# Performance work log

Hardware: AMD Instinct MI355X
Metric: run time of the kernel (lower is better)

The kernel has to match this reference:

```python
import jax, jax.numpy as jnp
import numpy as np

BLOCK = 16          # NVFP4 block size along contraction dim
FP4_MAX = 6.0       # max magnitude of E2M1
FP8_MAX = 448.0     # max magnitude of float8_e4m3fn

_LEVELS = jnp.array([0.0, 0.5, 1.0, 1.5, 2.0, 3.0, 4.0, 6.0], dtype=jnp.float32)
_MIDS   = jnp.array([0.25, 0.75, 1.25, 1.75, 2.5, 3.5, 5.0], dtype=jnp.float32)


def quantize_dequant_nvfp4(t, global_scale):
    """Fake-quantize t (last dim % 16 == 0) to NVFP4: per-16-block fp8-e4m3
    scale times global fp32 scale, values snapped to the E2M1 grid."""
    shp = t.shape
    tb = t.reshape(shp[:-1] + (shp[-1] // BLOCK, BLOCK))
    amax = jnp.max(jnp.abs(tb), axis=-1, keepdims=True)
    # per-block scale, quantized to float8_e4m3fn as in TensorCoreNVFP4Layout
    bs = amax / (FP4_MAX * global_scale)
    bs8 = bs.astype(jnp.float8_e4m3fn).astype(jnp.float32)
    scale = bs8 * global_scale                       # effective dequant scale
    v = tb / jnp.maximum(scale, 1e-12)
    sign = jnp.sign(v)
    a = jnp.clip(jnp.abs(v), 0.0, FP4_MAX)
    idx = jnp.sum(a[..., None] > _MIDS, axis=-1)     # nearest E2M1 level
    q = _LEVELS[idx] * sign * scale
    return q.reshape(shp)


def setup_inputs() -> dict:
    key = jax.random.key(0)
    kx, kw, kb = jax.random.split(key, 3)
    x = jax.random.normal(kx, (8192, 4096), dtype=jnp.float32)
    weight = jax.random.normal(kw, (4096, 4096), dtype=jnp.float32) * 0.02
    bias = jax.random.normal(kb, (4096,), dtype=jnp.float32) * 0.02
    # global scales (weight_scale_2 / input_scale): amax / (6 * 448)
    input_scale = jnp.max(jnp.abs(x)) / (FP4_MAX * FP8_MAX)
    weight_scale = jnp.max(jnp.abs(weight)) / (FP4_MAX * FP8_MAX)
    return {"x": x, "weight": weight, "bias": bias,
            "input_scale": input_scale, "weight_scale": weight_scale}


def reference(x, weight, bias, input_scale, weight_scale):
    xq = quantize_dequant_nvfp4(x, input_scale)      # [T, K]
    wq = quantize_dequant_nvfp4(weight, weight_scale)  # [N, K]
    return jnp.einsum('tk,nk->tn', xq, wq) + bias    # F.linear
```

## Files before the change

kernel.cpp:

```cpp
#include <hip/hip_runtime.h>
#include <hip/hip_bf16.h>
#include <stdint.h>

typedef __attribute__((ext_vector_type(8))) __bf16 bf16x8;
typedef __attribute__((ext_vector_type(4))) float f32x4;
typedef __attribute__((ext_vector_type(4))) unsigned int u32x4;

#define BM 256
#define BN 256
#define BKT 32
#define RING 4
#define SLOT_BYTES 16384


__device__ __forceinline__ float fp8_e4m3_rne(float x) {
  if (x < 0.015625f) {
    return rintf(x * 512.0f) * 0.001953125f;
  }
  uint32_t u = __float_as_uint(x);
  uint32_t keep = u & 0xFFF00000u;
  uint32_t rem  = u & 0x000FFFFFu;
  uint32_t lsb  = (u >> 20) & 1u;
  if (rem > 0x80000u || (rem == 0x80000u && lsb)) keep += 0x100000u;
  return __uint_as_float(keep);
}

__device__ __forceinline__ float snap_lvl(float a) {
  if (a > 5.0f)  return 6.0f;
  if (a > 3.5f)  return 4.0f;
  if (a > 2.5f)  return 3.0f;
  if (a > 1.75f) return 2.0f;
  if (a > 1.25f) return 1.5f;
  if (a > 0.75f) return 1.0f;
  if (a > 0.25f) return 0.5f;
  return 0.0f;
}

__global__ __launch_bounds__(256) void quant_nvfp4(
    const float* __restrict__ in, unsigned short* __restrict__ out,
    const float* __restrict__ gsp, int nblk) {
  int b = blockIdx.x * 256 + threadIdx.x;
  if (b >= nblk) return;
  float gs = gsp[0];
  const float4* p = reinterpret_cast<const float4*>(in) + (size_t)b * 4;
  float v[16];
#pragma unroll
  for (int i = 0; i < 4; ++i) {
    float4 t4 = p[i];
    v[i * 4 + 0] = t4.x; v[i * 4 + 1] = t4.y;
    v[i * 4 + 2] = t4.z; v[i * 4 + 3] = t4.w;
  }
  float amax = 0.0f;
#pragma unroll
  for (int i = 0; i < 16; ++i) amax = fmaxf(amax, fabsf(v[i]));
  float bs8 = fp8_e4m3_rne(amax / (6.0f * gs));
  float scale = fmaxf(bs8 * gs, 1e-12f);
  unsigned short o[16];
#pragma unroll
  for (int i = 0; i < 16; ++i) {
    float q = v[i] / scale;
    float a = fminf(fabsf(q), 6.0f);
    float val = copysignf(snap_lvl(a) * bs8, q);
    o[i] = (unsigned short)(__float_as_uint(val) >> 16);
  }
  uint4 w0 = make_uint4((uint32_t)o[0] | ((uint32_t)o[1] << 16),
                        (uint32_t)o[2] | ((uint32_t)o[3] << 16),
                        (uint32_t)o[4] | ((uint32_t)o[5] << 16),
                        (uint32_t)o[6] | ((uint32_t)o[7] << 16));
  uint4 w1 = make_uint4((uint32_t)o[8]  | ((uint32_t)o[9]  << 16),
                        (uint32_t)o[10] | ((uint32_t)o[11] << 16),
                        (uint32_t)o[12] | ((uint32_t)o[13] << 16),
                        (uint32_t)o[14] | ((uint32_t)o[15] << 16));
  uint4* op = reinterpret_cast<uint4*>(out + (size_t)b * 16);
  op[0] = w0;
  op[1] = w1;
}


__device__ __forceinline__ void async_lds16(const void* g, void* l) {
  __builtin_amdgcn_global_load_lds((__attribute__((address_space(1))) void*)(g),
                                   (__attribute__((address_space(3))) void*)(l),
                                   16, 0, 0);
}

#define DSR(dst, a) asm volatile("ds_read_b128 %0, %1" : "=v"(dst) : "v"(a))
#define LGKM(N) do { asm volatile("s_waitcnt lgkmcnt(" #N ")" ::: "memory"); \
                     __builtin_amdgcn_sched_barrier(0); } while (0)
#define BCB(x) __builtin_bit_cast(bf16x8, x)

#define MF4(mi, ar) do {                                                       \
    acc[mi][0] = __builtin_amdgcn_mfma_f32_16x16x32_bf16(BCB(ar), BCB(rb0), acc[mi][0], 0, 0, 0); \
    acc[mi][1] = __builtin_amdgcn_mfma_f32_16x16x32_bf16(BCB(ar), BCB(rb1), acc[mi][1], 0, 0, 0); \
    acc[mi][2] = __builtin_amdgcn_mfma_f32_16x16x32_bf16(BCB(ar), BCB(rb2), acc[mi][2], 0, 0, 0); \
    acc[mi][3] = __builtin_amdgcn_mfma_f32_16x16x32_bf16(BCB(ar), BCB(rb3), acc[mi][3], 0, 0, 0); \
  } while (0)

#define TILE(T, DO_STAGE, VMWAIT) do {                                         \
    const unsigned soff = (unsigned)(((T) & 3) * SLOT_BYTES);                  \
    VMWAIT;                                                                    \
    __builtin_amdgcn_s_barrier();                                              \
    if (DO_STAGE) {                                                            \
      char* _la = (char*)As + (((T) + 3) & 3) * SLOT_BYTES;                    \
      char* _lb = (char*)Bs + (((T) + 3) & 3) * SLOT_BYTES;                    \
      async_lds16(pA0 + (size_t)((T) + 3) * BKT, _la + lo0);                   \
      async_lds16(pB0 + (size_t)((T) + 3) * BKT, _lb + lo0);                   \
      async_lds16(pA1 + (size_t)((T) + 3) * BKT, _la + lo1);                   \
      async_lds16(pB1 + (size_t)((T) + 3) * BKT, _lb + lo1);                   \
    }                                                                          \
    u32x4 rb0, rb1, rb2, rb3, ra0, ra1, ra2, ra3, ra4, ra5, ra6, ra7;          \
    DSR(rb0, adB[0] + soff); DSR(rb1, adB[1] + soff);                          \
    DSR(rb2, adB[2] + soff); DSR(rb3, adB[3] + soff);                          \
    DSR(ra0, adA[0] + soff); DSR(ra1, adA[1] + soff);                          \
    DSR(ra2, adA[2] + soff); DSR(ra3, adA[3] + soff);                          \
    __builtin_amdgcn_sched_barrier(0);                                         \
    LGKM(3); __builtin_amdgcn_s_setprio(1); MF4(0, ra0);                       \
    LGKM(2); MF4(1, ra1);                                                      \
    __builtin_amdgcn_sched_barrier(0);                                         \
    DSR(ra4, adA[4] + soff); DSR(ra5, adA[5] + soff);                          \
    DSR(ra6, adA[6] + soff); DSR(ra7, adA[7] + soff);                          \
    __builtin_amdgcn_sched_barrier(0);                                         \
    LGKM(5); MF4(2, ra2);                                                      \
    LGKM(4); MF4(3, ra3);                                                      \
    LGKM(3); MF4(4, ra4);                                                      \
    LGKM(2); MF4(5, ra5);                                                      \
    LGKM(1); MF4(6, ra6);                                                      \
    LGKM(0); MF4(7, ra7);                                                      \
    __builtin_amdgcn_s_setprio(0);                                             \
    __builtin_amdgcn_sched_barrier(0);                                         \
  } while (0)

#define STAGE_TILE(s) {                                                        \
    char* _la = (char*)As + ((s) & 3) * SLOT_BYTES;                            \
    char* _lb = (char*)Bs + ((s) & 3) * SLOT_BYTES;                            \
    async_lds16(pA0 + (size_t)(s) * BKT, _la + lo0);                           \
    async_lds16(pB0 + (size_t)(s) * BKT, _lb + lo0);                           \
    async_lds16(pA1 + (size_t)(s) * BKT, _la + lo1);                           \
    async_lds16(pB1 + (size_t)(s) * BKT, _lb + lo1);                           \
  }

__global__ __launch_bounds__(512, 2) void gemm_bt_bf16(
    const unsigned short* __restrict__ A, const unsigned short* __restrict__ B,
    const float* __restrict__ bias, const float* __restrict__ gsx,
    const float* __restrict__ gsw, float* __restrict__ C,
    int M, int N, int K) {
  __shared__ __align__(16) unsigned short As[RING * 8192];
  __shared__ __align__(16) unsigned short Bs[RING * 8192];

  const int t = threadIdx.x;
  const int l = t & 63;
  const int w = t >> 6;
  const int wm = w >> 2, wn = w & 3;

  const int nbn = N / BN;
  const int nwg = (M / BM) * nbn;
  const int cpx = nwg >> 3;
  int bid = blockIdx.x;
  int logical = (bid & 7) * cpx + (bid >> 3);
  const int bm = logical / nbn, bn = logical % nbn;
  const int brow = bm * BM, bcol = bn * BN;

  unsigned int b0 = (unsigned int)t * 16u;
  unsigned int b1 = b0 + 8192u;
  unsigned int bp0 = b0 ^ (((b0 >> 7) & 3u) << 4);
  unsigned int bp1 = b1 ^ (((b1 >> 7) & 3u) << 4);
  const unsigned int lo0 = b0, lo1 = b1;
  const unsigned short* pA0 = A + (size_t)(brow + (bp0 >> 6)) * K + ((bp0 & 63u) >> 1);
  const unsigned short* pA1 = A + (size_t)(brow + (bp1 >> 6)) * K + ((bp1 & 63u) >> 1);
  const unsigned short* pB0 = B + (size_t)(bcol + (bp0 >> 6)) * K + ((bp0 & 63u) >> 1);
  const unsigned short* pB1 = B + (size_t)(bcol + (bp1 >> 6)) * K + ((bp1 & 63u) >> 1);

  const unsigned baseAu = (unsigned)(uintptr_t)(&As[0]);
  const unsigned baseBu = (unsigned)(uintptr_t)(&Bs[0]);
  unsigned int adA[8], adB[4];
#pragma unroll
  for (int mi = 0; mi < 8; ++mi) {
    unsigned int r = wm * 128 + mi * 16 + (l & 15);
    unsigned int q = r * 64 + ((l >> 4) << 4);
    adA[mi] = baseAu + (q ^ (((q >> 7) & 3u) << 4));
  }
#pragma unroll
  for (int ni = 0; ni < 4; ++ni) {
    unsigned int r = wn * 64 + ni * 16 + (l & 15);
    unsigned int q = r * 64 + ((l >> 4) << 4);
    adB[ni] = baseBu + (q ^ (((q >> 7) & 3u) << 4));
  }

  f32x4 acc[8][4] = {};

  const int nsub = K / BKT;

  STAGE_TILE(0);
  STAGE_TILE(1);
  STAGE_TILE(2);

#pragma unroll 1
  for (int T = 0; T < nsub - 3; ++T) {
    TILE(T, 1, asm volatile("s_waitcnt vmcnt(8)" ::: "memory"));
  }
  TILE(nsub - 3, 0, asm volatile("s_waitcnt vmcnt(8)" ::: "memory"));
  TILE(nsub - 2, 0, asm volatile("s_waitcnt vmcnt(4)" ::: "memory"));
  TILE(nsub - 1, 0, asm volatile("s_waitcnt vmcnt(0)" ::: "memory"));

  const float gscale = gsx[0] * gsw[0];
  float bias_r[4];
#pragma unroll
  for (int ni = 0; ni < 4; ++ni)
    bias_r[ni] = bias[bcol + wn * 64 + ni * 16 + (l & 15)];
#pragma unroll
  for (int mi = 0; mi < 8; ++mi) {
#pragma unroll
    for (int ni = 0; ni < 4; ++ni) {
#pragma unroll
      for (int r = 0; r < 4; ++r) {
        int row = brow + wm * 128 + mi * 16 + (l >> 4) * 4 + r;
        int col = bcol + wn * 64 + ni * 16 + (l & 15);
        C[(size_t)row * N + col] = acc[mi][ni][r] * gscale + bias_r[ni];
      }
    }
  }
}


extern "C" void kernel_launch(void* const* d_in, const int* in_sizes, int n_in,
                              void* d_out, int out_size, void* d_ws, size_t ws_size,
                              hipStream_t stream) {
  const float* x    = (const float*)d_in[0];
  const float* wgt  = (const float*)d_in[1];
  const float* bias = (const float*)d_in[2];
  const float* isc  = (const float*)d_in[3];
  const float* wsc  = (const float*)d_in[4];
  float* out = (float*)d_out;

  const int N = in_sizes[2];
  const int K = in_sizes[1] / N;
  const int M = in_sizes[0] / K;

  unsigned short* Aq = (unsigned short*)d_ws;
  unsigned short* Bq = Aq + (size_t)M * K;

  int nblkA = M * K / 16;
  quant_nvfp4<<<(nblkA + 255) / 256, 256, 0, stream>>>(x, Aq, isc, nblkA);
  int nblkB = N * K / 16;
  quant_nvfp4<<<(nblkB + 255) / 256, 256, 0, stream>>>(wgt, Bq, wsc, nblkB);

  dim3 grid((M / BM) * (N / BN));
  gemm_bt_bf16<<<grid, 512, 0, stream>>>(Aq, Bq, bias, isc, wsc, out, M, N, K);
}
```

Before: 290.8 us.

## Process two K-tiles per barrier with a five-slot LDS ring

Replaces the four-slot, one-tile-per-barrier main loop with a five-slot LDS ring where each barrier window stages two new tiles and computes two K sub-tiles, interleaving LDS reads of the second tile with MFMAs of the first. This halves the number of workgroup barriers and gives deeper software prefetch overlap. It raises LDS use to 320 KB-equivalent slots (160 KB per block), which may cut occupancy below the requested two blocks per CU. It also hardcodes K=4096 through the fixed trip count of 62 windows.

```diff
diff --git a/kernel.cpp b/kernel.cpp
--- a/kernel.cpp
+++ b/kernel.cpp
@@ -9,8 +9,7 @@
 #define BM 256
 #define BN 256
 #define BKT 32
-#define RING 4
-#define SLOT_BYTES 16384
+#define SLOT 16384
 
 
 __device__ __forceinline__ float fp8_e4m3_rne(float x) {
@@ -88,63 +87,71 @@
                      __builtin_amdgcn_sched_barrier(0); } while (0)
 #define BCB(x) __builtin_bit_cast(bf16x8, x)
 
-#define MF4(mi, ar) do {                                                       \
-    acc[mi][0] = __builtin_amdgcn_mfma_f32_16x16x32_bf16(BCB(ar), BCB(rb0), acc[mi][0], 0, 0, 0); \
-    acc[mi][1] = __builtin_amdgcn_mfma_f32_16x16x32_bf16(BCB(ar), BCB(rb1), acc[mi][1], 0, 0, 0); \
-    acc[mi][2] = __builtin_amdgcn_mfma_f32_16x16x32_bf16(BCB(ar), BCB(rb2), acc[mi][2], 0, 0, 0); \
-    acc[mi][3] = __builtin_amdgcn_mfma_f32_16x16x32_bf16(BCB(ar), BCB(rb3), acc[mi][3], 0, 0, 0); \
+#define MF4(mi, ar, b0, b1, b2, b3) do {                                       \
+    acc[mi][0] = __builtin_amdgcn_mfma_f32_16x16x32_bf16(BCB(ar), BCB(b0), acc[mi][0], 0, 0, 0); \
+    acc[mi][1] = __builtin_amdgcn_mfma_f32_16x16x32_bf16(BCB(ar), BCB(b1), acc[mi][1], 0, 0, 0); \
+    acc[mi][2] = __builtin_amdgcn_mfma_f32_16x16x32_bf16(BCB(ar), BCB(b2), acc[mi][2], 0, 0, 0); \
+    acc[mi][3] = __builtin_amdgcn_mfma_f32_16x16x32_bf16(BCB(ar), BCB(b3), acc[mi][3], 0, 0, 0); \
   } while (0)
 
-#define TILE(T, DO_STAGE, VMWAIT) do {                                         \
-    const unsigned soff = (unsigned)(((T) & 3) * SLOT_BYTES);                  \
-    VMWAIT;                                                                    \
+#define STAGE(tile, soff) {                                                    \
+    char* _la = (char*)As + (soff);                                            \
+    char* _lb = (char*)Bs + (soff);                                            \
+    async_lds16(pA0 + (size_t)(tile) * BKT, _la + lo0);                        \
+    async_lds16(pB0 + (size_t)(tile) * BKT, _lb + lo0);                        \
+    async_lds16(pA1 + (size_t)(tile) * BKT, _la + lo1);                        \
+    async_lds16(pB1 + (size_t)(tile) * BKT, _lb + lo1);                        \
+  }
+
+#define WINDOW(VMSTR, ta, oa, ob, o3, o4, DO3, DO4) do {                       \
+    u32x4 rb0, rb1, rb2, rb3, ra0, ra1, ra2, ra3, ra4, ra5, ra6, ra7;          \
+    u32x4 qb0, qb1, qb2, qb3, qa0, qa1, qa2, qa3, qa4, qa5, qa6, qa7;          \
+    asm volatile("s_waitcnt vmcnt(" VMSTR ")" ::: "memory");                   \
     __builtin_amdgcn_s_barrier();                                              \
-    if (DO_STAGE) {                                                            \
-      char* _la = (char*)As + (((T) + 3) & 3) * SLOT_BYTES;                    \
-      char* _lb = (char*)Bs + (((T) + 3) & 3) * SLOT_BYTES;                    \
-      async_lds16(pA0 + (size_t)((T) + 3) * BKT, _la + lo0);                   \
-      async_lds16(pB0 + (size_t)((T) + 3) * BKT, _lb + lo0);                   \
-      async_lds16(pA1 + (size_t)((T) + 3) * BKT, _la + lo1);                   \
-      async_lds16(pB1 + (size_t)((T) + 3) * BKT, _lb + lo1);                   \
-    }                                                                          \
-    u32x4 rb0, rb1, rb2, rb3, ra0, ra1, ra2, ra3, ra4, ra5, ra6, ra7;          \
-    DSR(rb0, adB[0] + soff); DSR(rb1, adB[1] + soff);                          \
-    DSR(rb2, adB[2] + soff); DSR(rb3, adB[3] + soff);                          \
-    DSR(ra0, adA[0] + soff); DSR(ra1, adA[1] + soff);                          \
-    DSR(ra2, adA[2] + soff); DSR(ra3, adA[3] + soff);                          \
-    __builtin_amdgcn_sched_barrier(0);                                         \
-    LGKM(3); __builtin_amdgcn_s_setprio(1); MF4(0, ra0);                       \
-    LGKM(2); MF4(1, ra1);                                                      \
-    __builtin_amdgcn_sched_barrier(0);                                         \
-    DSR(ra4, adA[4] + soff); DSR(ra5, adA[5] + soff);                          \
-    DSR(ra6, adA[6] + soff); DSR(ra7, adA[7] + soff);                          \
-    __builtin_amdgcn_sched_barrier(0);                                         \
-    LGKM(5); MF4(2, ra2);                                                      \
-    LGKM(4); MF4(3, ra3);                                                      \
-    LGKM(3); MF4(4, ra4);                                                      \
-    LGKM(2); MF4(5, ra5);                                                      \
-    LGKM(1); MF4(6, ra6);                                                      \
-    LGKM(0); MF4(7, ra7);                                                      \
+    if (DO3) STAGE((ta) + 3, o3);                                              \
+    if (DO4) STAGE((ta) + 4, o4);                                              \
+    DSR(rb0, adB[0] + (oa)); DSR(rb1, adB[1] + (oa));                          \
+    DSR(rb2, adB[2] + (oa)); DSR(rb3, adB[3] + (oa));                          \
+    DSR(ra0, adA[0] + (oa)); DSR(ra1, adA[1] + (oa));                          \
+    DSR(ra2, adA[2] + (oa)); DSR(ra3, adA[3] + (oa));                          \
+    DSR(ra4, adA[4] + (oa)); DSR(ra5, adA[5] + (oa));                          \
+    DSR(ra6, adA[6] + (oa)); DSR(ra7, adA[7] + (oa));                          \
+    __builtin_amdgcn_sched_barrier(0);                                         \
+    LGKM(7); __builtin_amdgcn_s_setprio(1); MF4(0, ra0, rb0, rb1, rb2, rb3);   \
+    LGKM(6); MF4(1, ra1, rb0, rb1, rb2, rb3);                                  \
+    LGKM(5); MF4(2, ra2, rb0, rb1, rb2, rb3);                                  \
+    LGKM(4); MF4(3, ra3, rb0, rb1, rb2, rb3);                                  \
+    LGKM(3); MF4(4, ra4, rb0, rb1, rb2, rb3);                                  \
+    DSR(qb0, adB[0] + (ob)); DSR(qb1, adB[1] + (ob));                          \
+    DSR(qb2, adB[2] + (ob)); DSR(qb3, adB[3] + (ob));                          \
+    DSR(qa0, adA[0] + (ob)); DSR(qa1, adA[1] + (ob));                          \
+    DSR(qa2, adA[2] + (ob)); DSR(qa3, adA[3] + (ob));                          \
+    __builtin_amdgcn_sched_barrier(0);                                         \
+    LGKM(10); MF4(5, ra5, rb0, rb1, rb2, rb3);                                 \
+    LGKM(9);  MF4(6, ra6, rb0, rb1, rb2, rb3);                                 \
+    LGKM(8);  MF4(7, ra7, rb0, rb1, rb2, rb3);                                 \
+    DSR(qa4, adA[4] + (ob)); DSR(qa5, adA[5] + (ob));                          \
+    DSR(qa6, adA[6] + (ob)); DSR(qa7, adA[7] + (ob));                          \
+    __builtin_amdgcn_sched_barrier(0);                                         \
+    LGKM(7); MF4(0, qa0, qb0, qb1, qb2, qb3);                                  \
+    LGKM(6); MF4(1, qa1, qb0, qb1, qb2, qb3);                                  \
+    LGKM(5); MF4(2, qa2, qb0, qb1, qb2, qb3);                                  \
+    LGKM(4); MF4(3, qa3, qb0, qb1, qb2, qb3);                                  \
+    LGKM(3); MF4(4, qa4, qb0, qb1, qb2, qb3);                                  \
+    LGKM(2); MF4(5, qa5, qb0, qb1, qb2, qb3);                                  \
+    LGKM(1); MF4(6, qa6, qb0, qb1, qb2, qb3);                                  \
+    LGKM(0); MF4(7, qa7, qb0, qb1, qb2, qb3);                                  \
     __builtin_amdgcn_s_setprio(0);                                             \
     __builtin_amdgcn_sched_barrier(0);                                         \
   } while (0)
-
-#define STAGE_TILE(s) {                                                        \
-    char* _la = (char*)As + ((s) & 3) * SLOT_BYTES;                            \
-    char* _lb = (char*)Bs + ((s) & 3) * SLOT_BYTES;                            \
-    async_lds16(pA0 + (size_t)(s) * BKT, _la + lo0);                           \
-    async_lds16(pB0 + (size_t)(s) * BKT, _lb + lo0);                           \
-    async_lds16(pA1 + (size_t)(s) * BKT, _la + lo1);                           \
-    async_lds16(pB1 + (size_t)(s) * BKT, _lb + lo1);                           \
-  }
 
 __global__ __launch_bounds__(512, 2) void gemm_bt_bf16(
     const unsigned short* __restrict__ A, const unsigned short* __restrict__ B,
     const float* __restrict__ bias, const float* __restrict__ gsx,
     const float* __restrict__ gsw, float* __restrict__ C,
     int M, int N, int K) {
-  __shared__ __align__(16) unsigned short As[RING * 8192];
-  __shared__ __align__(16) unsigned short Bs[RING * 8192];
+  __shared__ __align__(16) unsigned short As[5 * 8192];
+  __shared__ __align__(16) unsigned short Bs[5 * 8192];
 
   const int t = threadIdx.x;
   const int l = t & 63;
@@ -187,19 +194,22 @@
 
   f32x4 acc[8][4] = {};
 
-  const int nsub = K / BKT;
-
-  STAGE_TILE(0);
-  STAGE_TILE(1);
-  STAGE_TILE(2);
-
+  STAGE(0, 0);
+  STAGE(1, SLOT);
+  STAGE(2, 2 * SLOT);
+
+  int sa = 0;
 #pragma unroll 1
-  for (int T = 0; T < nsub - 3; ++T) {
-    TILE(T, 1, asm volatile("s_waitcnt vmcnt(8)" ::: "memory"));
-  }
-  TILE(nsub - 3, 0, asm volatile("s_waitcnt vmcnt(8)" ::: "memory"));
-  TILE(nsub - 2, 0, asm volatile("s_waitcnt vmcnt(4)" ::: "memory"));
-  TILE(nsub - 1, 0, asm volatile("s_waitcnt vmcnt(0)" ::: "memory"));
+  for (int k = 0; k < 62; ++k) {
+    int ta = 2 * k;
+    int sb = sa + 1; if (sb >= 5) sb -= 5;
+    int s3 = sa + 3; if (s3 >= 5) s3 -= 5;
+    int s4 = sa + 4; if (s4 >= 5) s4 -= 5;
+    WINDOW("4", ta, sa * SLOT, sb * SLOT, s3 * SLOT, s4 * SLOT, 1, 1);
+    sa += 2; if (sa >= 5) sa -= 5;
+  }
+  WINDOW("4", 124, 4 * SLOT, 0 * SLOT, 2 * SLOT, 0, 1, 0);
+  WINDOW("0", 126, 1 * SLOT, 2 * SLOT, 0, 0, 0, 0);
 
   const float gscale = gsx[0] * gsw[0];
   float bias_r[4];
```

Result: faster. 282.1 us (-3.0%).

## Switch GEMM main loop to 32x32x16 bf16 MFMA with five-slot LDS ring

Applied to the files above, without the earlier changes.

Replaces the 16x16x32 MFMA tiling (8x4 accumulators per wave) with 32x32x16 MFMA instructions (8 f32x16 accumulators), remapping LDS read addresses and the epilogue output row/col mapping. This cuts the number of MFMA issues per tile. The LDS ring grows from 4 to 5 slots while keeping a prefetch distance of 3, with slot indices tracked by a rolling counter. The K loop count is hardcoded to 125 iterations, which assumes K=4096. The larger LDS footprint may constrain occupancy.

```diff
diff --git a/kernel.cpp b/kernel.cpp
--- a/kernel.cpp
+++ b/kernel.cpp
@@ -3,14 +3,13 @@
 #include <stdint.h>
 
 typedef __attribute__((ext_vector_type(8))) __bf16 bf16x8;
-typedef __attribute__((ext_vector_type(4))) float f32x4;
+typedef __attribute__((ext_vector_type(16))) float f32x16;
 typedef __attribute__((ext_vector_type(4))) unsigned int u32x4;
 
 #define BM 256
 #define BN 256
 #define BKT 32
-#define RING 4
-#define SLOT_BYTES 16384
+#define SLOT 16384
 
 
 __device__ __forceinline__ float fp8_e4m3_rne(float x) {
@@ -86,65 +85,57 @@
 #define DSR(dst, a) asm volatile("ds_read_b128 %0, %1" : "=v"(dst) : "v"(a))
 #define LGKM(N) do { asm volatile("s_waitcnt lgkmcnt(" #N ")" ::: "memory"); \
                      __builtin_amdgcn_sched_barrier(0); } while (0)
+#define VMC(S) asm volatile("s_waitcnt vmcnt(" S ")" ::: "memory")
 #define BCB(x) __builtin_bit_cast(bf16x8, x)
 
-#define MF4(mi, ar) do {                                                       \
-    acc[mi][0] = __builtin_amdgcn_mfma_f32_16x16x32_bf16(BCB(ar), BCB(rb0), acc[mi][0], 0, 0, 0); \
-    acc[mi][1] = __builtin_amdgcn_mfma_f32_16x16x32_bf16(BCB(ar), BCB(rb1), acc[mi][1], 0, 0, 0); \
-    acc[mi][2] = __builtin_amdgcn_mfma_f32_16x16x32_bf16(BCB(ar), BCB(rb2), acc[mi][2], 0, 0, 0); \
-    acc[mi][3] = __builtin_amdgcn_mfma_f32_16x16x32_bf16(BCB(ar), BCB(rb3), acc[mi][3], 0, 0, 0); \
+#define MF2(i0, i1, ar, bx, by) do {                                           \
+    acc[i0] = __builtin_amdgcn_mfma_f32_32x32x16_bf16(BCB(ar), BCB(bx), acc[i0], 0, 0, 0); \
+    acc[i1] = __builtin_amdgcn_mfma_f32_32x32x16_bf16(BCB(ar), BCB(by), acc[i1], 0, 0, 0); \
   } while (0)
 
-#define TILE(T, DO_STAGE, VMWAIT) do {                                         \
-    const unsigned soff = (unsigned)(((T) & 3) * SLOT_BYTES);                  \
-    VMWAIT;                                                                    \
-    __builtin_amdgcn_s_barrier();                                              \
-    if (DO_STAGE) {                                                            \
-      char* _la = (char*)As + (((T) + 3) & 3) * SLOT_BYTES;                    \
-      char* _lb = (char*)Bs + (((T) + 3) & 3) * SLOT_BYTES;                    \
-      async_lds16(pA0 + (size_t)((T) + 3) * BKT, _la + lo0);                   \
-      async_lds16(pB0 + (size_t)((T) + 3) * BKT, _lb + lo0);                   \
-      async_lds16(pA1 + (size_t)((T) + 3) * BKT, _la + lo1);                   \
-      async_lds16(pB1 + (size_t)((T) + 3) * BKT, _lb + lo1);                   \
-    }                                                                          \
-    u32x4 rb0, rb1, rb2, rb3, ra0, ra1, ra2, ra3, ra4, ra5, ra6, ra7;          \
-    DSR(rb0, adB[0] + soff); DSR(rb1, adB[1] + soff);                          \
-    DSR(rb2, adB[2] + soff); DSR(rb3, adB[3] + soff);                          \
-    DSR(ra0, adA[0] + soff); DSR(ra1, adA[1] + soff);                          \
-    DSR(ra2, adA[2] + soff); DSR(ra3, adA[3] + soff);                          \
-    __builtin_amdgcn_sched_barrier(0);                                         \
-    LGKM(3); __builtin_amdgcn_s_setprio(1); MF4(0, ra0);                       \
-    LGKM(2); MF4(1, ra1);                                                      \
-    __builtin_amdgcn_sched_barrier(0);                                         \
-    DSR(ra4, adA[4] + soff); DSR(ra5, adA[5] + soff);                          \
-    DSR(ra6, adA[6] + soff); DSR(ra7, adA[7] + soff);                          \
-    __builtin_amdgcn_sched_barrier(0);                                         \
-    LGKM(5); MF4(2, ra2);                                                      \
-    LGKM(4); MF4(3, ra3);                                                      \
-    LGKM(3); MF4(4, ra4);                                                      \
-    LGKM(2); MF4(5, ra5);                                                      \
-    LGKM(1); MF4(6, ra6);                                                      \
-    LGKM(0); MF4(7, ra7);                                                      \
-    __builtin_amdgcn_s_setprio(0);                                             \
-    __builtin_amdgcn_sched_barrier(0);                                         \
-  } while (0)
-
-#define STAGE_TILE(s) {                                                        \
-    char* _la = (char*)As + ((s) & 3) * SLOT_BYTES;                            \
-    char* _lb = (char*)Bs + ((s) & 3) * SLOT_BYTES;                            \
+#define STAGE_TILE(s, so) {                                                    \
+    char* _la = (char*)As + (so);                                              \
+    char* _lb = (char*)Bs + (so);                                              \
     async_lds16(pA0 + (size_t)(s) * BKT, _la + lo0);                           \
     async_lds16(pB0 + (size_t)(s) * BKT, _lb + lo0);                           \
     async_lds16(pA1 + (size_t)(s) * BKT, _la + lo1);                           \
     async_lds16(pB1 + (size_t)(s) * BKT, _lb + lo1);                           \
   }
+
+#define TILE(VMSTR, soff, sStg, stgT, DO_S) do {                               \
+    u32x4 b00, b10, b01, b11, a0, a1, a2, a3, a4, a5, a6, a7;                  \
+    VMC(VMSTR);                                                                \
+    __builtin_amdgcn_s_barrier();                                              \
+    if (DO_S) { STAGE_TILE(stgT, sStg); }                                      \
+    DSR(b00, adB[0] + (soff)); DSR(b10, adB[1] + (soff));                      \
+    DSR(b01, adB[2] + (soff)); DSR(b11, adB[3] + (soff));                      \
+    DSR(a0, adA[0] + (soff));  DSR(a1, adA[1] + (soff));                       \
+    DSR(a2, adA[2] + (soff));  DSR(a3, adA[3] + (soff));                       \
+    __builtin_amdgcn_sched_barrier(0);                                         \
+    LGKM(3); __builtin_amdgcn_s_setprio(1);                                    \
+    MF2(0, 1, a0, b00, b10);                                                   \
+    LGKM(2); MF2(2, 3, a1, b00, b10);                                          \
+    __builtin_amdgcn_sched_barrier(0);                                         \
+    DSR(a4, adA[4] + (soff)); DSR(a5, adA[5] + (soff));                        \
+    DSR(a6, adA[6] + (soff)); DSR(a7, adA[7] + (soff));                        \
+    __builtin_amdgcn_sched_barrier(0);                                         \
+    LGKM(5); MF2(4, 5, a2, b00, b10);                                          \
+    LGKM(4); MF2(6, 7, a3, b00, b10);                                          \
+    LGKM(3); MF2(0, 1, a4, b01, b11);                                          \
+    LGKM(2); MF2(2, 3, a5, b01, b11);                                          \
+    LGKM(1); MF2(4, 5, a6, b01, b11);                                          \
+    LGKM(0); MF2(6, 7, a7, b01, b11);                                          \
+    __builtin_amdgcn_s_setprio(0);                                             \
+    __builtin_amdgcn_sched_barrier(0);                                         \
+  } while (0)
 
 __global__ __launch_bounds__(512, 2) void gemm_bt_bf16(
     const unsigned short* __restrict__ A, const unsigned short* __restrict__ B,
     const float* __restrict__ bias, const float* __restrict__ gsx,
     const float* __restrict__ gsw, float* __restrict__ C,
     int M, int N, int K) {
-  __shared__ __align__(16) unsigned short As[RING * 8192];
-  __shared__ __align__(16) unsigned short Bs[RING * 8192];
+  __shared__ __align__(16) unsigned short As[5 * 8192];
+  __shared__ __align__(16) unsigned short Bs[5 * 8192];
 
   const int t = threadIdx.x;
   const int l = t & 63;
@@ -173,48 +164,54 @@
   const unsigned baseBu = (unsigned)(uintptr_t)(&Bs[0]);
   unsigned int adA[8], adB[4];
 #pragma unroll
-  for (int mi = 0; mi < 8; ++mi) {
-    unsigned int r = wm * 128 + mi * 16 + (l & 15);
-    unsigned int q = r * 64 + ((l >> 4) << 4);
-    adA[mi] = baseAu + (q ^ (((q >> 7) & 3u) << 4));
-  }
-#pragma unroll
-  for (int ni = 0; ni < 4; ++ni) {
-    unsigned int r = wn * 64 + ni * 16 + (l & 15);
-    unsigned int q = r * 64 + ((l >> 4) << 4);
-    adB[ni] = baseBu + (q ^ (((q >> 7) & 3u) << 4));
-  }
-
-  f32x4 acc[8][4] = {};
-
-  const int nsub = K / BKT;
-
-  STAGE_TILE(0);
-  STAGE_TILE(1);
-  STAGE_TILE(2);
-
+  for (int mi = 0; mi < 4; ++mi) {
+    unsigned int r = (unsigned)wm * 128u + (unsigned)mi * 32u + ((unsigned)l & 31u);
+    unsigned int q0 = r * 64u + (((unsigned)l >> 5) << 4);
+    unsigned int q1 = q0 + 32u;
+    adA[mi]     = baseAu + (q0 ^ (((q0 >> 7) & 3u) << 4));
+    adA[4 + mi] = baseAu + (q1 ^ (((q1 >> 7) & 3u) << 4));
+  }
+#pragma unroll
+  for (int ni = 0; ni < 2; ++ni) {
+    unsigned int r = (unsigned)wn * 64u + (unsigned)ni * 32u + ((unsigned)l & 31u);
+    unsigned int q0 = r * 64u + (((unsigned)l >> 5) << 4);
+    unsigned int q1 = q0 + 32u;
+    adB[ni]     = baseBu + (q0 ^ (((q0 >> 7) & 3u) << 4));
+    adB[2 + ni] = baseBu + (q1 ^ (((q1 >> 7) & 3u) << 4));
+  }
+
+  f32x16 acc[8] = {};
+
+  STAGE_TILE(0, 0);
+  STAGE_TILE(1, SLOT);
+  STAGE_TILE(2, 2 * SLOT);
+
+  int sa = 0;
 #pragma unroll 1
-  for (int T = 0; T < nsub - 3; ++T) {
-    TILE(T, 1, asm volatile("s_waitcnt vmcnt(8)" ::: "memory"));
-  }
-  TILE(nsub - 3, 0, asm volatile("s_waitcnt vmcnt(8)" ::: "memory"));
-  TILE(nsub - 2, 0, asm volatile("s_waitcnt vmcnt(4)" ::: "memory"));
-  TILE(nsub - 1, 0, asm volatile("s_waitcnt vmcnt(0)" ::: "memory"));
+  for (int T = 0; T < 125; ++T) {
+    int s3 = sa + 3; if (s3 >= 5) s3 -= 5;
+    TILE("8", sa * SLOT, s3 * SLOT, T + 3, 1);
+    ++sa; if (sa == 5) sa = 0;
+  }
+  TILE("8", 0 * SLOT, 0, 0, 0);
+  TILE("4", 1 * SLOT, 0, 0, 0);
+  TILE("0", 2 * SLOT, 0, 0, 0);
 
   const float gscale = gsx[0] * gsw[0];
-  float bias_r[4];
-#pragma unroll
-  for (int ni = 0; ni < 4; ++ni)
-    bias_r[ni] = bias[bcol + wn * 64 + ni * 16 + (l & 15)];
-#pragma unroll
-  for (int mi = 0; mi < 8; ++mi) {
-#pragma unroll
-    for (int ni = 0; ni < 4; ++ni) {
-#pragma unroll
-      for (int r = 0; r < 4; ++r) {
-        int row = brow + wm * 128 + mi * 16 + (l >> 4) * 4 + r;
-        int col = bcol + wn * 64 + ni * 16 + (l & 15);
-        C[(size_t)row * N + col] = acc[mi][ni][r] * gscale + bias_r[ni];
+  float bias_r[2];
+#pragma unroll
+  for (int ni = 0; ni < 2; ++ni)
+    bias_r[ni] = bias[bcol + wn * 64 + ni * 32 + (l & 31)];
+#pragma unroll
+  for (int mi = 0; mi < 4; ++mi) {
+#pragma unroll
+    for (int ni = 0; ni < 2; ++ni) {
+      f32x16 v = acc[mi * 2 + ni];
+      int col = bcol + wn * 64 + ni * 32 + (l & 31);
+#pragma unroll
+      for (int r = 0; r < 16; ++r) {
+        int row = brow + wm * 128 + mi * 32 + (r & 3) + 8 * (r >> 2) + 4 * (l >> 5);
+        C[(size_t)row * N + col] = v[r] * gscale + bias_r[ni];
       }
     }
   }
```

New measurement: 306.6 us. 5.4% more time.

## Restructure GEMM main loop into barrier-separated half-tile phases with split staging

Applied to the files above, without the earlier changes.

Replaces the per-tile loop, which had a single barrier and interleaved lgkmcnt waits, with a ping-pong schedule. Each K-subtile is split into two phases: the low four A rows and the high four A rows. Each phase issues its LDS reads and half of the next tile's global->LDS loads, then hits a workgroup barrier, waits for all LDS reads and runs 16 MFMAs at raised priority. The intent is to keep waves in lockstep so memory and MFMA work from the two resident workgroups interleave better. The trip count is hardcoded for K=4096 (128 subtiles), and adding two barriers per phase may add stall overhead.

```diff
diff --git a/kernel.cpp b/kernel.cpp
--- a/kernel.cpp
+++ b/kernel.cpp
@@ -9,8 +9,7 @@
 #define BM 256
 #define BN 256
 #define BKT 32
-#define RING 4
-#define SLOT_BYTES 16384
+#define SLOT 16384
 
 
 __device__ __forceinline__ float fp8_e4m3_rne(float x) {
@@ -84,67 +83,62 @@
 }
 
 #define DSR(dst, a) asm volatile("ds_read_b128 %0, %1" : "=v"(dst) : "v"(a))
-#define LGKM(N) do { asm volatile("s_waitcnt lgkmcnt(" #N ")" ::: "memory"); \
-                     __builtin_amdgcn_sched_barrier(0); } while (0)
+#define VMC(S) asm volatile("s_waitcnt vmcnt(" S ")" ::: "memory")
 #define BCB(x) __builtin_bit_cast(bf16x8, x)
 
 #define MF4(mi, ar) do {                                                       \
-    acc[mi][0] = __builtin_amdgcn_mfma_f32_16x16x32_bf16(BCB(ar), BCB(rb0), acc[mi][0], 0, 0, 0); \
-    acc[mi][1] = __builtin_amdgcn_mfma_f32_16x16x32_bf16(BCB(ar), BCB(rb1), acc[mi][1], 0, 0, 0); \
-    acc[mi][2] = __builtin_amdgcn_mfma_f32_16x16x32_bf16(BCB(ar), BCB(rb2), acc[mi][2], 0, 0, 0); \
-    acc[mi][3] = __builtin_amdgcn_mfma_f32_16x16x32_bf16(BCB(ar), BCB(rb3), acc[mi][3], 0, 0, 0); \
+    acc[mi][0] = __builtin_amdgcn_mfma_f32_16x16x32_bf16(BCB(ar), BCB(bT0), acc[mi][0], 0, 0, 0); \
+    acc[mi][1] = __builtin_amdgcn_mfma_f32_16x16x32_bf16(BCB(ar), BCB(bT1), acc[mi][1], 0, 0, 0); \
+    acc[mi][2] = __builtin_amdgcn_mfma_f32_16x16x32_bf16(BCB(ar), BCB(bT2), acc[mi][2], 0, 0, 0); \
+    acc[mi][3] = __builtin_amdgcn_mfma_f32_16x16x32_bf16(BCB(ar), BCB(bT3), acc[mi][3], 0, 0, 0); \
   } while (0)
 
-#define TILE(T, DO_STAGE, VMWAIT) do {                                         \
-    const unsigned soff = (unsigned)(((T) & 3) * SLOT_BYTES);                  \
-    VMWAIT;                                                                    \
-    __builtin_amdgcn_s_barrier();                                              \
-    if (DO_STAGE) {                                                            \
-      char* _la = (char*)As + (((T) + 3) & 3) * SLOT_BYTES;                    \
-      char* _lb = (char*)Bs + (((T) + 3) & 3) * SLOT_BYTES;                    \
-      async_lds16(pA0 + (size_t)((T) + 3) * BKT, _la + lo0);                   \
-      async_lds16(pB0 + (size_t)((T) + 3) * BKT, _lb + lo0);                   \
-      async_lds16(pA1 + (size_t)((T) + 3) * BKT, _la + lo1);                   \
-      async_lds16(pB1 + (size_t)((T) + 3) * BKT, _lb + lo1);                   \
-    }                                                                          \
-    u32x4 rb0, rb1, rb2, rb3, ra0, ra1, ra2, ra3, ra4, ra5, ra6, ra7;          \
-    DSR(rb0, adB[0] + soff); DSR(rb1, adB[1] + soff);                          \
-    DSR(rb2, adB[2] + soff); DSR(rb3, adB[3] + soff);                          \
-    DSR(ra0, adA[0] + soff); DSR(ra1, adA[1] + soff);                          \
-    DSR(ra2, adA[2] + soff); DSR(ra3, adA[3] + soff);                          \
-    __builtin_amdgcn_sched_barrier(0);                                         \
-    LGKM(3); __builtin_amdgcn_s_setprio(1); MF4(0, ra0);                       \
-    LGKM(2); MF4(1, ra1);                                                      \
-    __builtin_amdgcn_sched_barrier(0);                                         \
-    DSR(ra4, adA[4] + soff); DSR(ra5, adA[5] + soff);                          \
-    DSR(ra6, adA[6] + soff); DSR(ra7, adA[7] + soff);                          \
-    __builtin_amdgcn_sched_barrier(0);                                         \
-    LGKM(5); MF4(2, ra2);                                                      \
-    LGKM(4); MF4(3, ra3);                                                      \
-    LGKM(3); MF4(4, ra4);                                                      \
-    LGKM(2); MF4(5, ra5);                                                      \
-    LGKM(1); MF4(6, ra6);                                                      \
-    LGKM(0); MF4(7, ra7);                                                      \
+#define SG_A0(T_, SO) async_lds16(pA0 + (size_t)(T_) * BKT, (char*)As + (SO) + lo0)
+#define SG_B0(T_, SO) async_lds16(pB0 + (size_t)(T_) * BKT, (char*)Bs + (SO) + lo0)
+#define SG_A1(T_, SO) async_lds16(pA1 + (size_t)(T_) * BKT, (char*)As + (SO) + lo1)
+#define SG_B1(T_, SO) async_lds16(pB1 + (size_t)(T_) * BKT, (char*)Bs + (SO) + lo1)
+
+#define PH_LO(SOFF, STG, VMS) do {                                             \
+    DSR(bT0, adB[0] + (SOFF)); DSR(bT1, adB[1] + (SOFF));                      \
+    DSR(bT2, adB[2] + (SOFF)); DSR(bT3, adB[3] + (SOFF));                      \
+    DSR(aL0, adA[0] + (SOFF)); DSR(aL1, adA[1] + (SOFF));                      \
+    DSR(aL2, adA[2] + (SOFF)); DSR(aL3, adA[3] + (SOFF));                      \
+    STG;                                                                       \
+    VMS;                                                                       \
+    __builtin_amdgcn_sched_barrier(0);                                         \
+    __builtin_amdgcn_s_barrier();                                              \
+    asm volatile("s_waitcnt lgkmcnt(0)" ::: "memory");                         \
+    __builtin_amdgcn_sched_barrier(0);                                         \
+    __builtin_amdgcn_s_setprio(1);                                             \
+    MF4(0, aL0); MF4(1, aL1); MF4(2, aL2); MF4(3, aL3);                        \
     __builtin_amdgcn_s_setprio(0);                                             \
     __builtin_amdgcn_sched_barrier(0);                                         \
+    __builtin_amdgcn_s_barrier();                                              \
   } while (0)
 
-#define STAGE_TILE(s) {                                                        \
-    char* _la = (char*)As + ((s) & 3) * SLOT_BYTES;                            \
-    char* _lb = (char*)Bs + ((s) & 3) * SLOT_BYTES;                            \
-    async_lds16(pA0 + (size_t)(s) * BKT, _la + lo0);                           \
-    async_lds16(pB0 + (size_t)(s) * BKT, _lb + lo0);                           \
-    async_lds16(pA1 + (size_t)(s) * BKT, _la + lo1);                           \
-    async_lds16(pB1 + (size_t)(s) * BKT, _lb + lo1);                           \
-  }
+#define PH_HI(SOFF, STG, VMS) do {                                             \
+    DSR(aH0, adA[4] + (SOFF)); DSR(aH1, adA[5] + (SOFF));                      \
+    DSR(aH2, adA[6] + (SOFF)); DSR(aH3, adA[7] + (SOFF));                      \
+    STG;                                                                       \
+    VMS;                                                                       \
+    __builtin_amdgcn_sched_barrier(0);                                         \
+    __builtin_amdgcn_s_barrier();                                              \
+    asm volatile("s_waitcnt lgkmcnt(0)" ::: "memory");                         \
+    __builtin_amdgcn_sched_barrier(0);                                         \
+    __builtin_amdgcn_s_setprio(1);                                             \
+    MF4(4, aH0); MF4(5, aH1); MF4(6, aH2); MF4(7, aH3);                        \
+    __builtin_amdgcn_s_setprio(0);                                             \
+    __builtin_amdgcn_sched_barrier(0);                                         \
+    __builtin_amdgcn_s_barrier();                                              \
+  } while (0)
 
 __global__ __launch_bounds__(512, 2) void gemm_bt_bf16(
     const unsigned short* __restrict__ A, const unsigned short* __restrict__ B,
     const float* __restrict__ bias, const float* __restrict__ gsx,
     const float* __restrict__ gsw, float* __restrict__ C,
     int M, int N, int K) {
-  __shared__ __align__(16) unsigned short As[RING * 8192];
-  __shared__ __align__(16) unsigned short Bs[RING * 8192];
+  __shared__ __align__(16) unsigned short As[4 * 8192];
+  __shared__ __align__(16) unsigned short Bs[4 * 8192];
 
   const int t = threadIdx.x;
   const int l = t & 63;
@@ -186,20 +180,35 @@
   }
 
   f32x4 acc[8][4] = {};
-
-  const int nsub = K / BKT;
-
-  STAGE_TILE(0);
-  STAGE_TILE(1);
-  STAGE_TILE(2);
+  u32x4 aL0, aL1, aL2, aL3, aH0, aH1, aH2, aH3, bT0, bT1, bT2, bT3;
+
+  SG_A0(0, 0);        SG_B0(0, 0);        SG_A1(0, 0);        SG_B1(0, 0);
+  SG_A0(1, SLOT);     SG_B0(1, SLOT);     SG_A1(1, SLOT);     SG_B1(1, SLOT);
+  SG_A0(2, 2 * SLOT); SG_B0(2, 2 * SLOT); SG_A1(2, 2 * SLOT); SG_B1(2, 2 * SLOT);
+  VMC("8");
+  __builtin_amdgcn_s_barrier();
 
 #pragma unroll 1
-  for (int T = 0; T < nsub - 3; ++T) {
-    TILE(T, 1, asm volatile("s_waitcnt vmcnt(8)" ::: "memory"));
-  }
-  TILE(nsub - 3, 0, asm volatile("s_waitcnt vmcnt(8)" ::: "memory"));
-  TILE(nsub - 2, 0, asm volatile("s_waitcnt vmcnt(4)" ::: "memory"));
-  TILE(nsub - 1, 0, asm volatile("s_waitcnt vmcnt(0)" ::: "memory"));
+  for (int i = 0; i < 62; ++i) {
+    const int base = (i & 1) * 2;
+    const int s0 = base * SLOT;
+    const int s1 = s0 + SLOT;
+    const int sX = (base ^ 3) * SLOT;
+    const int sY = s0;
+    const int X = 2 * i + 3, Y = 2 * i + 4;
+    PH_LO(s0, { SG_A0(X, sX); SG_B0(X, sX); }, (void)0);
+    PH_HI(s0, { SG_A1(X, sX); SG_B1(X, sX); }, VMC("8"));
+    PH_LO(s1, { SG_A0(Y, sY); SG_B0(Y, sY); }, (void)0);
+    PH_HI(s1, { SG_A1(Y, sY); SG_B1(Y, sY); }, VMC("8"));
+  }
+  PH_LO(0, { SG_A0(127, 3 * SLOT); SG_B0(127, 3 * SLOT); }, (void)0);
+  PH_HI(0, { SG_A1(127, 3 * SLOT); SG_B1(127, 3 * SLOT); }, VMC("8"));
+  PH_LO(SLOT, {}, (void)0);
+  PH_HI(SLOT, {}, VMC("4"));
+  PH_LO(2 * SLOT, {}, VMC("0"));
+  PH_HI(2 * SLOT, {}, (void)0);
+  PH_LO(3 * SLOT, {}, (void)0);
+  PH_HI(3 * SLOT, {}, (void)0);
 
   const float gscale = gsx[0] * gsw[0];
   float bias_r[4];
```

Result: no change. 291.7 us (+0.3%).
